# Optimization experiments

Measured on AMD Instinct MI355X. Metric: run time of the kernel, lower is better.

Reference implementation:

```python
import jax, jax.numpy as jnp
import numpy as np

B, S, D, H = 4, 1024, 1024, 16
HD = D // H  # 64
NEG = -10000000.0


def setup_inputs() -> dict:
    key = jax.random.key(0)
    ks = jax.random.split(key, 8)
    x = jax.random.normal(ks[0], (B, S, D), dtype=jnp.float32)
    adj = jax.random.randint(ks[1], (B, S, S), 0, 2).astype(jnp.float32)
    scale = 1.0 / np.sqrt(D)
    Wq = jax.random.normal(ks[2], (D, D), dtype=jnp.float32) * scale
    bq = jnp.zeros((D,), dtype=jnp.float32)
    Wk = jax.random.normal(ks[3], (D, D), dtype=jnp.float32) * scale
    bk = jnp.zeros((D,), dtype=jnp.float32)
    Wv = jax.random.normal(ks[4], (D, D), dtype=jnp.float32) * scale
    bv = jnp.zeros((D,), dtype=jnp.float32)
    return {"x": x, "adj": adj, "Wq": Wq, "bq": bq, "Wk": Wk, "bk": bk, "Wv": Wv, "bv": bv}


def reference(x, adj, Wq, bq, Wk, bk, Wv, bv):
    # QKV projections, split into heads: [B,S,D] -> [B,H,S,HD]
    def heads(t):
        return t.reshape(B, S, H, HD).transpose(0, 2, 1, 3)

    q = heads(x @ Wq + bq)
    k = heads(x @ Wk + bk)
    v = heads(x @ Wv + bv)

    # scaled scores [B,H,S,S]
    scores = jnp.einsum('bhqd,bhkd->bhqk', q, k) / jnp.sqrt(jnp.asarray(HD, x.dtype))
    # adjacency mask: 0 where adj>=0.5 else -1e7, broadcast over heads
    mask_add = jnp.where(adj < 0.5, jnp.asarray(NEG, x.dtype), jnp.asarray(0.0, x.dtype))
    scores = scores + mask_add[:, None, :, :]

    probs = jax.nn.softmax(scores, axis=-1)
    ctx = jnp.einsum('bhqk,bhkd->bhqd', probs, v)  # [B,H,S,HD]
    ctx = ctx.transpose(0, 2, 1, 3).reshape(B, S, D)
    h = jax.nn.relu(ctx)
    return (h, adj)
```

## Files before the change

kernel.cpp:

```cpp
#include <hip/hip_runtime.h>

constexpr int Bn  = 4;
constexpr int Sn  = 1024;
constexpr int Dn  = 1024;
constexpr int Hn  = 16;
constexpr int HDn = 64;

using short8  = __attribute__((ext_vector_type(8))) short;
using float4v = __attribute__((ext_vector_type(4))) float;

__device__ __forceinline__ ushort f2bf(float f) {
    union { float f; unsigned u; } v; v.f = f;
    unsigned r = v.u + 0x7fff + ((v.u >> 16) & 1);
    return (ushort)(r >> 16);
}

__device__ __forceinline__ void gload16(const void* g, void* l) {
    __builtin_amdgcn_global_load_lds(
        (const __attribute__((address_space(1))) void*)g,
        (__attribute__((address_space(3))) void*)l, 16, 0, 0);
}

__global__ __launch_bounds__(256) void convert_x(const float* __restrict__ x,
                                                 ushort* __restrict__ xb)
{
    const size_t i = ((size_t)blockIdx.x * 256 + threadIdx.x) * 8;
    float4 a = *(const float4*)&x[i];
    float4 b = *(const float4*)&x[i + 4];
    ushort o[8] = {f2bf(a.x), f2bf(a.y), f2bf(a.z), f2bf(a.w),
                   f2bf(b.x), f2bf(b.y), f2bf(b.z), f2bf(b.w)};
    *(uint4*)&xb[i] = *(const uint4*)o;
}

__global__ __launch_bounds__(256) void transpose_w(
    const float* __restrict__ Wq, const float* __restrict__ Wk,
    const float* __restrict__ Wv, ushort* __restrict__ Wt)
{
    const int which = blockIdx.z;
    const float* __restrict__ W = (which == 0) ? Wq : (which == 1) ? Wk : Wv;
    ushort* __restrict__ O = Wt + (size_t)which * Dn * Dn;

    const int k0 = blockIdx.x * 64;
    const int n0 = blockIdx.y * 64;
    const int t  = threadIdx.x;

    __shared__ __align__(16) ushort T[64][72];

    const int kl = t >> 4;
    const int nl = (t & 15) * 4;
#pragma unroll
    for (int p = 0; p < 4; ++p) {
        float4 w = *(const float4*)&W[(size_t)(k0 + p * 16 + kl) * Dn + n0 + nl];
        T[nl + 0][p * 16 + kl] = f2bf(w.x);
        T[nl + 1][p * 16 + kl] = f2bf(w.y);
        T[nl + 2][p * 16 + kl] = f2bf(w.z);
        T[nl + 3][p * 16 + kl] = f2bf(w.w);
    }
    __syncthreads();
    const int nr = t >> 2;
    const int kc = (t & 3) * 16;
    uint4 u0 = *(const uint4*)&T[nr][kc];
    uint4 u1 = *(const uint4*)&T[nr][kc + 8];
    *(uint4*)&O[(size_t)(n0 + nr) * Dn + k0 + kc]     = u0;
    *(uint4*)&O[(size_t)(n0 + nr) * Dn + k0 + kc + 8] = u1;
}

__global__ __launch_bounds__(256) void build_mask(const float* __restrict__ adj,
                                                  ushort* __restrict__ Mw)
{
    const int qt = blockIdx.x, kt = blockIdx.y, b = blockIdx.z;
    const int tid = threadIdx.x;

    __shared__ ushort msk[128][68];

    const float* ap = adj + ((size_t)b * Sn + qt * 128) * Sn + kt * 64;
#pragma unroll
    for (int c = 0; c < 8; ++c) {
        const int e = tid + 256 * c, row = e >> 4, c4 = (e & 15) * 4;
        float4 a = *(const float4*)&ap[(size_t)row * Sn + c4];
        ushort m[4] = {(ushort)(a.x < 0.5f ? 0xCB19 : 0), (ushort)(a.y < 0.5f ? 0xCB19 : 0),
                       (ushort)(a.z < 0.5f ? 0xCB19 : 0), (ushort)(a.w < 0.5f ? 0xCB19 : 0)};
        *(uint2*)&msk[row][c4] = *(const uint2*)m;
    }
    __syncthreads();

    const int w = tid >> 6, g = (tid >> 4) & 3, ml = tid & 15;
    ushort u[32];
#pragma unroll
    for (int mt = 0; mt < 4; ++mt)
#pragma unroll
        for (int j = 0; j < 2; ++j)
#pragma unroll
            for (int r = 0; r < 4; ++r)
                u[(mt * 2 + j) * 4 + r] = msk[w * 32 + j * 16 + ml][mt * 16 + g * 4 + r];

    ushort* dst = Mw + (((((size_t)((b * 8 + qt) * 16 + kt)) * 4 + w) * 4 + g) * 16 + ml) * 32;
#pragma unroll
    for (int c = 0; c < 4; ++c)
        *(uint4*)&dst[c * 8] = ((const uint4*)u)[c];
}

__global__ __launch_bounds__(256) void qkv_gemm(
    const ushort* __restrict__ xb, const ushort* __restrict__ Wt,
    const float* __restrict__ bq, const float* __restrict__ bk,
    const float* __restrict__ bv,
    ushort* __restrict__ Qb, ushort* __restrict__ Kb, ushort* __restrict__ Vb)
{
    const int which = blockIdx.z;
    const ushort* __restrict__ Bw   = Wt + (size_t)which * Dn * Dn;
    const float* __restrict__  bias = (which == 0) ? bq : (which == 1) ? bk : bv;
    ushort* __restrict__       Out  = (which == 0) ? Qb : (which == 1) ? Kb : Vb;
    const float scale = (which == 0) ? 0.125f : 1.0f;

    const int n0   = blockIdx.x * 128;
    const int m0   = blockIdx.y * 128;
    const int tid  = threadIdx.x;
    const int wave = tid >> 6;
    const int lane = tid & 63;
    const int wm   = wave >> 1;
    const int wn   = wave & 1;

    __shared__ __align__(16) ushort As[128 * 32];
    __shared__ __align__(16) ushort Bs[128 * 32];

    const int L0 = wave * 64 + lane;
    const int r0s = L0 >> 2, c0s = (L0 & 3) * 8;
    const int L1 = L0 + 256;
    const int r1s = L1 >> 2, c1s = (L1 & 3) * 8;

    const ushort* pA0 = &xb[(size_t)(m0 + r0s) * Dn + c0s];
    const ushort* pA1 = &xb[(size_t)(m0 + r1s) * Dn + c1s];
    const ushort* pB0 = &Bw[(size_t)(n0 + r0s) * Dn + c0s];
    const ushort* pB1 = &Bw[(size_t)(n0 + r1s) * Dn + c1s];

    char* ldsA0 = (char*)As + wave * 1024;
    char* ldsA1 = (char*)As + wave * 1024 + 4096;
    char* ldsB0 = (char*)Bs + wave * 1024;
    char* ldsB1 = (char*)Bs + wave * 1024 + 4096;

    const int mlane = lane & 15;
    const int kg    = (lane >> 4) * 8;

    float4v acc[4][4];
    const float4v z4 = {0.f, 0.f, 0.f, 0.f};
#pragma unroll
    for (int i = 0; i < 4; ++i)
#pragma unroll
        for (int j = 0; j < 4; ++j) acc[i][j] = z4;

    for (int k0 = 0; k0 < Dn; k0 += 32) {
        __syncthreads();
        gload16(pA0, ldsA0);
        gload16(pA1, ldsA1);
        gload16(pB0, ldsB0);
        gload16(pB1, ldsB1);
        pA0 += 32; pA1 += 32; pB0 += 32; pB1 += 32;
        __syncthreads();

        short8 af[4], bf[4];
#pragma unroll
        for (int i = 0; i < 4; ++i)
            af[i] = *(const short8*)&As[(wm * 64 + i * 16 + mlane) * 32 + kg];
#pragma unroll
        for (int j = 0; j < 4; ++j)
            bf[j] = *(const short8*)&Bs[(wn * 64 + j * 16 + mlane) * 32 + kg];
#pragma unroll
        for (int i = 0; i < 4; ++i)
#pragma unroll
            for (int j = 0; j < 4; ++j)
                acc[i][j] = __builtin_amdgcn_mfma_f32_16x16x32_bf16(af[i], bf[j], acc[i][j], 0, 0, 0);
    }

    const int rb  = (lane >> 4) * 4;
    const int col = lane & 15;
#pragma unroll
    for (int j = 0; j < 4; ++j) {
        const int n  = n0 + wn * 64 + j * 16 + col;
        const float bias_n = bias[n];
        const int h  = n >> 6;
        const int hd = n & 63;
#pragma unroll
        for (int i = 0; i < 4; ++i) {
#pragma unroll
            for (int r = 0; r < 4; ++r) {
                const int m = m0 + wm * 64 + i * 16 + rb + r;
                const int b = m >> 10;
                const int s = m & 1023;
                size_t addr;
                if (which == 2)
                    addr = (((size_t)(b * Hn + h)) * HDn + hd) * Sn + s;
                else
                    addr = (((size_t)(b * Hn + h)) * Sn + s) * HDn + hd;
                Out[addr] = f2bf((acc[i][j][r] + bias_n) * scale);
            }
        }
    }
}

__global__ __launch_bounds__(256, 2) void attn_mfma(
    const ushort* __restrict__ Q, const ushort* __restrict__ K,
    const ushort* __restrict__ Vt, const ushort* __restrict__ Mw,
    float* __restrict__ out)
{
    const int qt = blockIdx.x, h = blockIdx.y, b = blockIdx.z;
    const int tid = threadIdx.x;
    const int w = tid >> 6, lane = tid & 63;
    const int ml = lane & 15, g = lane >> 4, kg = g * 8;

    const size_t hb = ((size_t)(b * Hn + h)) * Sn * HDn;
    const ushort* Kg = K + hb;
    const ushort* Vg = Vt + hb;

    __shared__ __align__(16) ushort Ks[2 * 64 * 32];
    __shared__ __align__(16) ushort Vs[2 * 64 * 32];
    __shared__ __align__(16) ushort Pb[2 * 128 * 40];

    short8 bq[2][2];
#pragma unroll
    for (int kp = 0; kp < 2; ++kp)
#pragma unroll
        for (int j = 0; j < 2; ++j)
            bq[kp][j] = *(const short8*)&Q[hb + (size_t)(qt * 128 + w * 32 + j * 16 + ml) * HDn
                                           + kp * 32 + kg];

    const float4v z4 = {0.f, 0.f, 0.f, 0.f};
    float4v acc[4][2];
#pragma unroll
    for (int mt = 0; mt < 4; ++mt)
#pragma unroll
        for (int j = 0; j < 2; ++j) acc[mt][j] = z4;
    float ls[2] = {0.f, 0.f};

    for (int kt = 0; kt < 16; ++kt) {
        __syncthreads();
#pragma unroll
        for (int p = 0; p < 2; ++p) {
            const int e = tid + 256 * p, row = e >> 3, cc = e & 7;
            uint4 k4 = *(const uint4*)&Kg[(size_t)(kt * 64 + row) * HDn + cc * 8];
            *(uint4*)&Ks[(cc >> 2) * 2048 + row * 32 + (cc & 3) * 8] = k4;
            uint4 v4 = *(const uint4*)&Vg[(size_t)row * Sn + kt * 64 + cc * 8];
            *(uint4*)&Vs[(cc >> 2) * 2048 + row * 32 + (cc & 3) * 8] = v4;
        }

        const ushort* mp = Mw + (((((size_t)((b * 8 + qt) * 16 + kt)) * 4 + w) * 4 + g) * 16 + ml) * 32;
        union { uint4 v[4]; ushort u[32]; } mk;
        mk.v[0] = *(const uint4*)&mp[0];
        mk.v[1] = *(const uint4*)&mp[8];
        mk.v[2] = *(const uint4*)&mp[16];
        mk.v[3] = *(const uint4*)&mp[24];

        float4v s_[4][2];
#pragma unroll
        for (int mt = 0; mt < 4; ++mt)
#pragma unroll
            for (int j = 0; j < 2; ++j)
#pragma unroll
                for (int r = 0; r < 4; ++r)
                    s_[mt][j][r] = __uint_as_float((unsigned)mk.u[(mt * 2 + j) * 4 + r] << 16);

        __syncthreads();

#pragma unroll
        for (int kp = 0; kp < 2; ++kp)
#pragma unroll
            for (int mt = 0; mt < 4; ++mt) {
                short8 ak = *(const short8*)&Ks[kp * 2048 + (mt * 16 + ml) * 32 + kg];
                s_[mt][0] = __builtin_amdgcn_mfma_f32_16x16x32_bf16(ak, bq[kp][0], s_[mt][0], 0, 0, 0);
                s_[mt][1] = __builtin_amdgcn_mfma_f32_16x16x32_bf16(ak, bq[kp][1], s_[mt][1], 0, 0, 0);
            }

#pragma unroll
        for (int mt = 0; mt < 4; ++mt)
#pragma unroll
            for (int j = 0; j < 2; ++j) {
                const float p0 = __expf(s_[mt][j][0]);
                const float p1 = __expf(s_[mt][j][1]);
                const float p2 = __expf(s_[mt][j][2]);
                const float p3 = __expf(s_[mt][j][3]);
                ls[j] += (p0 + p1) + (p2 + p3);
                uint2 d;
                d.x = (unsigned)f2bf(p0) | ((unsigned)f2bf(p1) << 16);
                d.y = (unsigned)f2bf(p2) | ((unsigned)f2bf(p3) << 16);
                *(uint2*)&Pb[(mt >> 1) * 5120 + (w * 32 + j * 16 + ml) * 40 + (mt & 1) * 16 + g * 4] = d;
            }

#pragma unroll
        for (int kp = 0; kp < 2; ++kp) {
            short8 bp0 = *(const short8*)&Pb[kp * 5120 + (w * 32 + ml) * 40 + kg];
            short8 bp1 = *(const short8*)&Pb[kp * 5120 + (w * 32 + 16 + ml) * 40 + kg];
#pragma unroll
            for (int mt = 0; mt < 4; ++mt) {
                short8 av = *(const short8*)&Vs[kp * 2048 + (mt * 16 + ml) * 32 + kg];
                acc[mt][0] = __builtin_amdgcn_mfma_f32_16x16x32_bf16(av, bp0, acc[mt][0], 0, 0, 0);
                acc[mt][1] = __builtin_amdgcn_mfma_f32_16x16x32_bf16(av, bp1, acc[mt][1], 0, 0, 0);
            }
        }
    }

#pragma unroll
    for (int j = 0; j < 2; ++j) {
        float l = ls[j];
        l += __shfl_xor(l, 16, 64);
        l += __shfl_xor(l, 32, 64);
        const float inv = 1.0f / l;
        const int q = qt * 128 + w * 32 + j * 16 + ml;
#pragma unroll
        for (int mt = 0; mt < 4; ++mt) {
            float4 o;
            o.x = fmaxf(acc[mt][j][0] * inv, 0.0f);
            o.y = fmaxf(acc[mt][j][1] * inv, 0.0f);
            o.z = fmaxf(acc[mt][j][2] * inv, 0.0f);
            o.w = fmaxf(acc[mt][j][3] * inv, 0.0f);
            *(float4*)&out[((size_t)b * Sn + q) * Dn + h * 64 + mt * 16 + g * 4] = o;
        }
    }
}

extern "C" void kernel_launch(void* const* d_in, const int* in_sizes, int n_in,
                              void* d_out, int out_size, void* d_ws, size_t ws_size,
                              hipStream_t stream)
{
    const float* x   = (const float*)d_in[0];
    const float* adj = (const float*)d_in[1];
    const float* Wq  = (const float*)d_in[2];
    const float* bq  = (const float*)d_in[3];
    const float* Wk  = (const float*)d_in[4];
    const float* bk  = (const float*)d_in[5];
    const float* Wv  = (const float*)d_in[6];
    const float* bv  = (const float*)d_in[7];
    float* out = (float*)d_out;

    ushort* xb = (ushort*)d_ws;
    ushort* Wt = xb + (size_t)Bn * Sn * Dn;
    ushort* Qb = Wt + (size_t)3 * Dn * Dn;
    ushort* Kb = Qb + (size_t)Bn * Hn * Sn * HDn;
    ushort* Vb = Kb + (size_t)Bn * Hn * Sn * HDn;
    ushort* Mw = Vb + (size_t)Bn * Hn * Sn * HDn;

    convert_x<<<dim3((Bn * Sn * Dn) / (256 * 8)), 256, 0, stream>>>(x, xb);
    transpose_w<<<dim3(16, 16, 3), 256, 0, stream>>>(Wq, Wk, Wv, Wt);
    build_mask<<<dim3(8, 16, 4), 256, 0, stream>>>(adj, Mw);

    qkv_gemm<<<dim3(Dn / 128, (Bn * Sn) / 128, 3), 256, 0, stream>>>(
        xb, Wt, bq, bk, bv, Qb, Kb, Vb);

    attn_mfma<<<dim3(Sn / 128, Hn, Bn), 256, 0, stream>>>(Qb, Kb, Vb, Mw, out);

    hipMemcpyAsync(out + (size_t)Bn * Sn * Dn, adj,
                   (size_t)Bn * Sn * Sn * sizeof(float),
                   hipMemcpyDeviceToDevice, stream);
}
```

Measured before the change: 206.5 us.

## Rewrite attention with 32x32 MFMA, 256-query tiles, bitmask adjacency, register-prefetched K/V

```diff
diff --git a/kernel.cpp b/kernel.cpp
--- a/kernel.cpp
+++ b/kernel.cpp
@@ -6,8 +6,9 @@
 constexpr int Hn  = 16;
 constexpr int HDn = 64;
 
-using short8  = __attribute__((ext_vector_type(8))) short;
-using float4v = __attribute__((ext_vector_type(4))) float;
+using short8   = __attribute__((ext_vector_type(8))) short;
+using float4v  = __attribute__((ext_vector_type(4))) float;
+using float16v = __attribute__((ext_vector_type(16))) float;
 
 __device__ __forceinline__ ushort f2bf(float f) {
     union { float f; unsigned u; } v; v.f = f;
@@ -66,38 +67,32 @@
 }
 
 __global__ __launch_bounds__(256) void build_mask(const float* __restrict__ adj,
-                                                  ushort* __restrict__ Mw)
-{
-    const int qt = blockIdx.x, kt = blockIdx.y, b = blockIdx.z;
-    const int tid = threadIdx.x;
-
-    __shared__ ushort msk[128][68];
-
-    const float* ap = adj + ((size_t)b * Sn + qt * 128) * Sn + kt * 64;
-#pragma unroll
-    for (int c = 0; c < 8; ++c) {
-        const int e = tid + 256 * c, row = e >> 4, c4 = (e & 15) * 4;
-        float4 a = *(const float4*)&ap[(size_t)row * Sn + c4];
-        ushort m[4] = {(ushort)(a.x < 0.5f ? 0xCB19 : 0), (ushort)(a.y < 0.5f ? 0xCB19 : 0),
-                       (ushort)(a.z < 0.5f ? 0xCB19 : 0), (ushort)(a.w < 0.5f ? 0xCB19 : 0)};
-        *(uint2*)&msk[row][c4] = *(const uint2*)m;
-    }
-    __syncthreads();
-
-    const int w = tid >> 6, g = (tid >> 4) & 3, ml = tid & 15;
-    ushort u[32];
-#pragma unroll
-    for (int mt = 0; mt < 4; ++mt)
-#pragma unroll
-        for (int j = 0; j < 2; ++j)
-#pragma unroll
-            for (int r = 0; r < 4; ++r)
-                u[(mt * 2 + j) * 4 + r] = msk[w * 32 + j * 16 + ml][mt * 16 + g * 4 + r];
-
-    ushort* dst = Mw + (((((size_t)((b * 8 + qt) * 16 + kt)) * 4 + w) * 4 + g) * 16 + ml) * 32;
-#pragma unroll
-    for (int c = 0; c < 4; ++c)
-        *(uint4*)&dst[c * 8] = ((const uint4*)u)[c];
+                                                  uint2* __restrict__ Mb)
+{
+    const int rid  = blockIdx.x * 256 + threadIdx.x;
+    const int lane = rid & 63;
+    const int w    = (rid >> 6) & 3;
+    const int kt   = (rid >> 8) & 15;
+    const int qt   = (rid >> 12) & 3;
+    const int b    = rid >> 14;
+    const int col  = lane & 31, hi = lane >> 5;
+
+    unsigned bits[2] = {0u, 0u};
+#pragma unroll
+    for (int mt = 0; mt < 2; ++mt)
+#pragma unroll
+        for (int jt = 0; jt < 2; ++jt) {
+            const int q = qt * 256 + w * 64 + jt * 32 + col;
+            const float* row = adj + ((size_t)b * Sn + q) * Sn;
+#pragma unroll
+            for (int rg = 0; rg < 4; ++rg) {
+                float4 a = *(const float4*)&row[kt * 64 + mt * 32 + rg * 8 + hi * 4];
+                unsigned bb = (a.x >= 0.5f ? 1u : 0u) | (a.y >= 0.5f ? 2u : 0u) |
+                              (a.z >= 0.5f ? 4u : 0u) | (a.w >= 0.5f ? 8u : 0u);
+                bits[mt] |= bb << (jt * 16 + rg * 4);
+            }
+        }
+    Mb[rid] = make_uint2(bits[0], bits[1]);
 }
 
 __global__ __launch_bounds__(256) void qkv_gemm(
@@ -197,122 +192,146 @@
     }
 }
 
-__global__ __launch_bounds__(256, 2) void attn_mfma(
+__global__ __launch_bounds__(256, 1) void attn_mfma(
     const ushort* __restrict__ Q, const ushort* __restrict__ K,
-    const ushort* __restrict__ Vt, const ushort* __restrict__ Mw,
+    const ushort* __restrict__ Vt, const uint2* __restrict__ Mb,
     float* __restrict__ out)
 {
     const int qt = blockIdx.x, h = blockIdx.y, b = blockIdx.z;
-    const int tid = threadIdx.x;
-    const int w = tid >> 6, lane = tid & 63;
-    const int ml = lane & 15, g = lane >> 4, kg = g * 8;
+    const int tid  = threadIdx.x;
+    const int w    = tid >> 6, lane = tid & 63;
+    const int col  = lane & 31, hi = lane >> 5;
 
     const size_t hb = ((size_t)(b * Hn + h)) * Sn * HDn;
     const ushort* Kg = K + hb;
     const ushort* Vg = Vt + hb;
 
-    __shared__ __align__(16) ushort Ks[2 * 64 * 32];
-    __shared__ __align__(16) ushort Vs[2 * 64 * 32];
-    __shared__ __align__(16) ushort Pb[2 * 128 * 40];
-
-    short8 bq[2][2];
-#pragma unroll
-    for (int kp = 0; kp < 2; ++kp)
-#pragma unroll
-        for (int j = 0; j < 2; ++j)
-            bq[kp][j] = *(const short8*)&Q[hb + (size_t)(qt * 128 + w * 32 + j * 16 + ml) * HDn
-                                           + kp * 32 + kg];
-
-    const float4v z4 = {0.f, 0.f, 0.f, 0.f};
-    float4v acc[4][2];
-#pragma unroll
-    for (int mt = 0; mt < 4; ++mt)
-#pragma unroll
-        for (int j = 0; j < 2; ++j) acc[mt][j] = z4;
+    __shared__ __align__(16) ushort Ks[2][64 * 72];
+    __shared__ __align__(16) ushort Vs[2][64 * 72];
+
+    short8 qf[2][4];
+#pragma unroll
+    for (int jt = 0; jt < 2; ++jt)
+#pragma unroll
+        for (int kp = 0; kp < 4; ++kp)
+            qf[jt][kp] = *(const short8*)&Q[hb +
+                (size_t)(qt * 256 + w * 64 + jt * 32 + col) * HDn + kp * 16 + hi * 8];
+
+    float16v o_[2][2];
+#pragma unroll
+    for (int dt = 0; dt < 2; ++dt)
+#pragma unroll
+        for (int jt = 0; jt < 2; ++jt)
+#pragma unroll
+            for (int r = 0; r < 16; ++r) o_[dt][jt][r] = 0.f;
     float ls[2] = {0.f, 0.f};
 
+    const int c0 = tid, c1 = tid + 256;
+    const int la0 = (c0 >> 3) * 72 + (c0 & 7) * 8;
+    const int la1 = (c1 >> 3) * 72 + (c1 & 7) * 8;
+
+    uint4 k0 = *(const uint4*)&Kg[(size_t)(c0 >> 3) * HDn + (c0 & 7) * 8];
+    uint4 k1 = *(const uint4*)&Kg[(size_t)(c1 >> 3) * HDn + (c1 & 7) * 8];
+    uint4 v0 = *(const uint4*)&Vg[(size_t)(c0 >> 3) * Sn + (c0 & 7) * 8];
+    uint4 v1 = *(const uint4*)&Vg[(size_t)(c1 >> 3) * Sn + (c1 & 7) * 8];
+    *(uint4*)&Ks[0][la0] = k0;  *(uint4*)&Ks[0][la1] = k1;
+    *(uint4*)&Vs[0][la0] = v0;  *(uint4*)&Vs[0][la1] = v1;
+    __syncthreads();
+
+    const uint2* mbase = Mb + ((size_t)(((b * 4 + qt) * 16) * 4 + w)) * 64 + lane;
+
     for (int kt = 0; kt < 16; ++kt) {
+        const int cur = kt & 1;
+        if (kt < 15) {
+            k0 = *(const uint4*)&Kg[(size_t)((kt + 1) * 64 + (c0 >> 3)) * HDn + (c0 & 7) * 8];
+            k1 = *(const uint4*)&Kg[(size_t)((kt + 1) * 64 + (c1 >> 3)) * HDn + (c1 & 7) * 8];
+            v0 = *(const uint4*)&Vg[(size_t)(c0 >> 3) * Sn + (kt + 1) * 64 + (c0 & 7) * 8];
+            v1 = *(const uint4*)&Vg[(size_t)(c1 >> 3) * Sn + (kt + 1) * 64 + (c1 & 7) * 8];
+        }
+        const uint2 m = mbase[(size_t)kt * 256];
+
+#pragma unroll
+        for (int mt = 0; mt < 2; ++mt) {
+            float16v s_[2];
+#pragma unroll
+            for (int jt = 0; jt < 2; ++jt)
+#pragma unroll
+                for (int r = 0; r < 16; ++r) s_[jt][r] = 0.f;
+#pragma unroll
+            for (int kp = 0; kp < 4; ++kp) {
+                short8 ak = *(const short8*)&Ks[cur][(mt * 32 + col) * 72 + kp * 16 + hi * 8];
+                s_[0] = __builtin_amdgcn_mfma_f32_32x32x16_bf16(ak, qf[0][kp], s_[0], 0, 0, 0);
+                s_[1] = __builtin_amdgcn_mfma_f32_32x32x16_bf16(ak, qf[1][kp], s_[1], 0, 0, 0);
+            }
+
+            const unsigned mw = (mt == 0) ? m.x : m.y;
+            unsigned up[2][8];
+#pragma unroll
+            for (int jt = 0; jt < 2; ++jt) {
+                float p[16];
+#pragma unroll
+                for (int r = 0; r < 16; ++r) {
+                    const float e = __expf(s_[jt][r]);
+                    p[r] = ((mw >> (jt * 16 + r)) & 1u) ? e : 0.0f;
+                    ls[jt] += p[r];
+                }
+#pragma unroll
+                for (int pr = 0; pr < 8; ++pr)
+                    up[jt][pr] = (unsigned)f2bf(p[2 * pr]) | ((unsigned)f2bf(p[2 * pr + 1]) << 16);
+            }
+
+#pragma unroll
+            for (int kh = 0; kh < 2; ++kh) {
+                short8 pf[2];
+#pragma unroll
+                for (int jt = 0; jt < 2; ++jt) {
+                    const unsigned a0 = up[jt][kh * 4 + 0], a1 = up[jt][kh * 4 + 1];
+                    const unsigned a2 = up[jt][kh * 4 + 2], a3 = up[jt][kh * 4 + 3];
+                    const unsigned t0 = (unsigned)__shfl_xor((int)(hi ? a0 : a2), 32, 64);
+                    const unsigned t1 = (unsigned)__shfl_xor((int)(hi ? a1 : a3), 32, 64);
+                    union { short8 s; unsigned u[4]; } f;
+                    f.u[0] = hi ? t0 : a0;
+                    f.u[1] = hi ? t1 : a1;
+                    f.u[2] = hi ? a2 : t0;
+                    f.u[3] = hi ? a3 : t1;
+                    pf[jt] = f.s;
+                }
+                const int kp = mt * 2 + kh;
+#pragma unroll
+                for (int dt = 0; dt < 2; ++dt) {
+                    short8 av = *(const short8*)&Vs[cur][(dt * 32 + col) * 72 + kp * 16 + hi * 8];
+                    o_[dt][0] = __builtin_amdgcn_mfma_f32_32x32x16_bf16(av, pf[0], o_[dt][0], 0, 0, 0);
+                    o_[dt][1] = __builtin_amdgcn_mfma_f32_32x32x16_bf16(av, pf[1], o_[dt][1], 0, 0, 0);
+                }
+            }
+        }
+
+        if (kt < 15) {
+            const int nxt = cur ^ 1;
+            *(uint4*)&Ks[nxt][la0] = k0;  *(uint4*)&Ks[nxt][la1] = k1;
+            *(uint4*)&Vs[nxt][la0] = v0;  *(uint4*)&Vs[nxt][la1] = v1;
+        }
         __syncthreads();
-#pragma unroll
-        for (int p = 0; p < 2; ++p) {
-            const int e = tid + 256 * p, row = e >> 3, cc = e & 7;
-            uint4 k4 = *(const uint4*)&Kg[(size_t)(kt * 64 + row) * HDn + cc * 8];
-            *(uint4*)&Ks[(cc >> 2) * 2048 + row * 32 + (cc & 3) * 8] = k4;
-            uint4 v4 = *(const uint4*)&Vg[(size_t)row * Sn + kt * 64 + cc * 8];
-            *(uint4*)&Vs[(cc >> 2) * 2048 + row * 32 + (cc & 3) * 8] = v4;
-        }
-
-        const ushort* mp = Mw + (((((size_t)((b * 8 + qt) * 16 + kt)) * 4 + w) * 4 + g) * 16 + ml) * 32;
-        union { uint4 v[4]; ushort u[32]; } mk;
-        mk.v[0] = *(const uint4*)&mp[0];
-        mk.v[1] = *(const uint4*)&mp[8];
-        mk.v[2] = *(const uint4*)&mp[16];
-        mk.v[3] = *(const uint4*)&mp[24];
-
-        float4v s_[4][2];
-#pragma unroll
-        for (int mt = 0; mt < 4; ++mt)
-#pragma unroll
-            for (int j = 0; j < 2; ++j)
-#pragma unroll
-                for (int r = 0; r < 4; ++r)
-                    s_[mt][j][r] = __uint_as_float((unsigned)mk.u[(mt * 2 + j) * 4 + r] << 16);
-
-        __syncthreads();
-
-#pragma unroll
-        for (int kp = 0; kp < 2; ++kp)
-#pragma unroll
-            for (int mt = 0; mt < 4; ++mt) {
-                short8 ak = *(const short8*)&Ks[kp * 2048 + (mt * 16 + ml) * 32 + kg];
-                s_[mt][0] = __builtin_amdgcn_mfma_f32_16x16x32_bf16(ak, bq[kp][0], s_[mt][0], 0, 0, 0);
-                s_[mt][1] = __builtin_amdgcn_mfma_f32_16x16x32_bf16(ak, bq[kp][1], s_[mt][1], 0, 0, 0);
-            }
-
-#pragma unroll
-        for (int mt = 0; mt < 4; ++mt)
-#pragma unroll
-            for (int j = 0; j < 2; ++j) {
-                const float p0 = __expf(s_[mt][j][0]);
-                const float p1 = __expf(s_[mt][j][1]);
-                const float p2 = __expf(s_[mt][j][2]);
-                const float p3 = __expf(s_[mt][j][3]);
-                ls[j] += (p0 + p1) + (p2 + p3);
-                uint2 d;
-                d.x = (unsigned)f2bf(p0) | ((unsigned)f2bf(p1) << 16);
-                d.y = (unsigned)f2bf(p2) | ((unsigned)f2bf(p3) << 16);
-                *(uint2*)&Pb[(mt >> 1) * 5120 + (w * 32 + j * 16 + ml) * 40 + (mt & 1) * 16 + g * 4] = d;
-            }
-
-#pragma unroll
-        for (int kp = 0; kp < 2; ++kp) {
-            short8 bp0 = *(const short8*)&Pb[kp * 5120 + (w * 32 + ml) * 40 + kg];
-            short8 bp1 = *(const short8*)&Pb[kp * 5120 + (w * 32 + 16 + ml) * 40 + kg];
-#pragma unroll
-            for (int mt = 0; mt < 4; ++mt) {
-                short8 av = *(const short8*)&Vs[kp * 2048 + (mt * 16 + ml) * 32 + kg];
-                acc[mt][0] = __builtin_amdgcn_mfma_f32_16x16x32_bf16(av, bp0, acc[mt][0], 0, 0, 0);
-                acc[mt][1] = __builtin_amdgcn_mfma_f32_16x16x32_bf16(av, bp1, acc[mt][1], 0, 0, 0);
-            }
-        }
-    }
-
-#pragma unroll
-    for (int j = 0; j < 2; ++j) {
-        float l = ls[j];
-        l += __shfl_xor(l, 16, 64);
-        l += __shfl_xor(l, 32, 64);
+    }
+
+#pragma unroll
+    for (int jt = 0; jt < 2; ++jt) {
+        float l = ls[jt] + (float)__shfl_xor((float)ls[jt], 32, 64);
         const float inv = 1.0f / l;
-        const int q = qt * 128 + w * 32 + j * 16 + ml;
-#pragma unroll
-        for (int mt = 0; mt < 4; ++mt) {
-            float4 o;
-            o.x = fmaxf(acc[mt][j][0] * inv, 0.0f);
-            o.y = fmaxf(acc[mt][j][1] * inv, 0.0f);
-            o.z = fmaxf(acc[mt][j][2] * inv, 0.0f);
-            o.w = fmaxf(acc[mt][j][3] * inv, 0.0f);
-            *(float4*)&out[((size_t)b * Sn + q) * Dn + h * 64 + mt * 16 + g * 4] = o;
-        }
+        const int q = qt * 256 + w * 64 + jt * 32 + col;
+        float* op = &out[((size_t)b * Sn + q) * Dn + h * 64];
+#pragma unroll
+        for (int dt = 0; dt < 2; ++dt)
+#pragma unroll
+            for (int rg = 0; rg < 4; ++rg) {
+                const int d = dt * 32 + rg * 8 + hi * 4;
+                float4 o4;
+                o4.x = fmaxf(o_[dt][jt][rg * 4 + 0] * inv, 0.0f);
+                o4.y = fmaxf(o_[dt][jt][rg * 4 + 1] * inv, 0.0f);
+                o4.z = fmaxf(o_[dt][jt][rg * 4 + 2] * inv, 0.0f);
+                o4.w = fmaxf(o_[dt][jt][rg * 4 + 3] * inv, 0.0f);
+                *(float4*)&op[d] = o4;
+            }
     }
 }
 
@@ -335,16 +354,16 @@
     ushort* Qb = Wt + (size_t)3 * Dn * Dn;
     ushort* Kb = Qb + (size_t)Bn * Hn * Sn * HDn;
     ushort* Vb = Kb + (size_t)Bn * Hn * Sn * HDn;
-    ushort* Mw = Vb + (size_t)Bn * Hn * Sn * HDn;
+    uint2*  Mb = (uint2*)(Vb + (size_t)Bn * Hn * Sn * HDn);
 
     convert_x<<<dim3((Bn * Sn * Dn) / (256 * 8)), 256, 0, stream>>>(x, xb);
     transpose_w<<<dim3(16, 16, 3), 256, 0, stream>>>(Wq, Wk, Wv, Wt);
-    build_mask<<<dim3(8, 16, 4), 256, 0, stream>>>(adj, Mw);
+    build_mask<<<dim3((Bn * 4 * 16 * 4 * 64) / 256), 256, 0, stream>>>(adj, Mb);
 
     qkv_gemm<<<dim3(Dn / 128, (Bn * Sn) / 128, 3), 256, 0, stream>>>(
         xb, Wt, bq, bk, bv, Qb, Kb, Vb);
 
-    attn_mfma<<<dim3(Sn / 128, Hn, Bn), 256, 0, stream>>>(Qb, Kb, Vb, Mw, out);
+    attn_mfma<<<dim3(Sn / 256, Hn, Bn), 256, 0, stream>>>(Qb, Kb, Vb, Mb, out);
 
     hipMemcpyAsync(out + (size_t)Bn * Sn * Dn, adj,
                    (size_t)Bn * Sn * Sn * sizeof(float),
```

New measurement: 192.5 us. -6.8%, faster.
